# Performance work log

Hardware: AMD Instinct MI355X
Metric: run time of the kernel (lower is better)

Reference implementation:

```python
import jax, jax.numpy as jnp
import numpy as np

N = 50000
EPS = 1e-4
NUM_CLASSES = 10
PROTOS_PER_CLASS = 5


def setup_inputs() -> dict:
    key = jax.random.key(0)
    ks = jax.random.split(key, 12)
    x = jax.random.normal(ks[0], (N, 512), dtype=jnp.float32)
    edge_index = jax.random.randint(ks[1], (2, 640000), 0, N, dtype=jnp.int64)
    # GCNConv weights (PyG: y = x @ W^T + b after aggregation)
    def glorot(k, o, i):
        s = jnp.sqrt(6.0 / (o + i)).astype(jnp.float32)
        return jax.random.uniform(k, (o, i), jnp.float32, -s, s)
    W1 = glorot(ks[2], 128, 512); b1 = jnp.zeros((128,), jnp.float32)
    W2 = glorot(ks[3], 128, 128); b2 = jnp.zeros((128,), jnp.float32)
    W3 = glorot(ks[4], 128, 128); b3 = jnp.zeros((128,), jnp.float32)
    prototype_vectors = jax.random.uniform(ks[5], (NUM_CLASSES * PROTOS_PER_CLASS, 128), jnp.float32)
    # last layer: +1 for prototype's own class, -0.5 elsewhere, no bias
    proto_class = jnp.arange(NUM_CLASSES * PROTOS_PER_CLASS) // PROTOS_PER_CLASS  # [P]
    identity = (proto_class[None, :] == jnp.arange(NUM_CLASSES)[:, None]).astype(jnp.float32)  # [C,P]
    last_w = 1.0 * identity + (-0.5) * (1.0 - identity)
    return {"x": x, "edge_index": edge_index, "W1": W1, "b1": b1, "W2": W2,
            "b2": b2, "W3": W3, "b3": b3,
            "prototype_vectors": prototype_vectors, "last_w": last_w}


def _gcn_conv(h, src, dst, deg_inv_sqrt, W, b):
    # h: [N,Fin]; messages from src -> dst with symmetric norm; self-loops included in src/dst
    m = h @ W.T                                   # [N,Fout]
    norm = deg_inv_sqrt[src] * deg_inv_sqrt[dst]  # [E+N]
    out = jax.ops.segment_sum(norm[:, None] * m[src], dst, num_segments=N)
    return out + b


def reference(x, edge_index, W1, b1, W2, b2, W3, b3, prototype_vectors, last_w):
    # add self loops once; degree computed on targets (PyG gcn_norm)
    loop = jnp.arange(N, dtype=edge_index.dtype)
    src = jnp.concatenate([edge_index[0], loop])
    dst = jnp.concatenate([edge_index[1], loop])
    deg = jax.ops.segment_sum(jnp.ones_like(src, dtype=x.dtype), dst, num_segments=N)
    deg_inv_sqrt = jnp.where(deg > 0, jax.lax.rsqrt(deg), 0.0)

    h = jax.nn.relu(_gcn_conv(x, src, dst, deg_inv_sqrt, W1, b1))
    h = jax.nn.relu(_gcn_conv(h, src, dst, deg_inv_sqrt, W2, b2))
    h = jax.nn.relu(_gcn_conv(h, src, dst, deg_inv_sqrt, W3, b3))
    emb = h  # [N,128]

    xp = emb @ prototype_vectors.T                                    # [N,P]
    distance = (-2.0 * xp + jnp.sum(emb * emb, axis=1, keepdims=True)
                + jnp.sum(prototype_vectors * prototype_vectors, axis=1)[None, :])
    similarity = jnp.log((distance + 1.0) / (distance + EPS))         # [N,P]
    logits = similarity @ last_w.T                                    # [N,C]
    probs = jax.nn.softmax(logits, axis=-1)
    return logits, probs, emb, distance
```

## Files before the change

kernel.cpp:

```cpp
#include <hip/hip_runtime.h>
#include <cstdint>
#include <cstddef>

#define NFEAT 128
#define NPROTO 50
#define NCLS 10

typedef __attribute__((ext_vector_type(8))) short short8;
typedef __attribute__((ext_vector_type(4))) float floatx4;
typedef _Float16 halfv8 __attribute__((ext_vector_type(8)));


__device__ __forceinline__ void split1(float v, unsigned short& h, unsigned short& l) {
  unsigned int b = __float_as_uint(v);
  h = (unsigned short)(b >> 16);
  float r = v - __uint_as_float(b & 0xFFFF0000u);
  l = (unsigned short)(__float_as_uint(r) >> 16);
}


__global__ __launch_bounds__(256)
void prep_kernel(const float* __restrict__ W1, const float* __restrict__ W2,
                 const float* __restrict__ W3, const float* __restrict__ proto,
                 unsigned short* __restrict__ W1h, unsigned short* __restrict__ W1l,
                 unsigned short* __restrict__ W2h, unsigned short* __restrict__ W2l,
                 unsigned short* __restrict__ W3h, unsigned short* __restrict__ W3l,
                 unsigned short* __restrict__ Ph, unsigned short* __restrict__ Pl,
                 float* __restrict__ pn, int* __restrict__ zero_base, int zero_n) {
  int g = blockIdx.x * 256 + threadIdx.x;
  int stride = gridDim.x * 256;
  for (int i = g; i < 128 * 512; i += stride) {
    unsigned short h, l; split1(W1[i], h, l); W1h[i] = h; W1l[i] = l;
  }
  for (int i = g; i < 128 * 128; i += stride) {
    unsigned short h, l; split1(W2[i], h, l); W2h[i] = h; W2l[i] = l;
  }
  for (int i = g; i < 128 * 128; i += stride) {
    unsigned short h, l; split1(W3[i], h, l); W3h[i] = h; W3l[i] = l;
  }
  for (int i = g; i < 64 * 128; i += stride) {
    int p = i >> 7;
    float v = (p < NPROTO) ? proto[p * 128 + (i & 127)] : 0.f;
    unsigned short h, l; split1(v, h, l); Ph[i] = h; Pl[i] = l;
  }
  for (int i = g; i < zero_n; i += stride) zero_base[i] = 0;
  if (g < 64) {
    float s = 0.f;
    if (g < NPROTO)
      for (int f = 0; f < 128; ++f) { float v = proto[g * 128 + f]; s += v * v; }
    pn[g] = s;
  }
}


__global__ __launch_bounds__(256) void count_kernel(const int* __restrict__ dst,
                                                    int* __restrict__ cnt, int E) {
  int e = blockIdx.x * 256 + threadIdx.x;
  if (e < E) atomicAdd(&cnt[dst[e]], 1);
}


__global__ __launch_bounds__(256)
void scan_lb_kernel(const int* __restrict__ cnt, int* __restrict__ row_ptr,
                    float* __restrict__ dis,
                    unsigned long long* __restrict__ state, int Nn) {
  __shared__ int s[256];
  __shared__ int exc_s;
  int b = blockIdx.x;
  int t = threadIdx.x;
  int i = b * 256 + t;
  int v = (i < Nn) ? cnt[i] : 0;
  s[t] = v;
  __syncthreads();
#pragma unroll
  for (int off = 1; off < 256; off <<= 1) {
    int add = (t >= off) ? s[t - off] : 0;
    __syncthreads();
    s[t] += add;
    __syncthreads();
  }
  int tile_sum = s[255];
  if (t == 0) {
    unsigned long long pkt = (1ULL << 32) | (unsigned int)tile_sum;
    __hip_atomic_store(&state[b], pkt, __ATOMIC_RELEASE, __HIP_MEMORY_SCOPE_AGENT);
    if (b == 0) exc_s = 0;
  }
  if (b > 0 && t < 64) {
    int acc = 0;
    for (int p = t; p < b; p += 64) {
      unsigned long long pk;
      do {
        pk = __hip_atomic_load(&state[p], __ATOMIC_ACQUIRE, __HIP_MEMORY_SCOPE_AGENT);
      } while ((pk >> 32) == 0);
      acc += (int)(unsigned int)pk;
    }
#pragma unroll
    for (int off = 32; off; off >>= 1) acc += __shfl_down(acc, off);
    if (t == 0) exc_s = acc;
  }
  __syncthreads();
  int exc = exc_s;
  if (i < Nn) {
    row_ptr[i] = exc + s[t] - v;
    dis[i] = 1.0f / sqrtf((float)(v + 1));
  }
  if (b == gridDim.x - 1 && t == 0) row_ptr[Nn] = exc + tile_sum;
}

__global__ __launch_bounds__(256) void fill_kernel(const int* __restrict__ src,
                                                   const int* __restrict__ dst,
                                                   const int* __restrict__ row_ptr,
                                                   int* __restrict__ cursor,
                                                   int* __restrict__ csr_src, int E) {
  int e = blockIdx.x * 256 + threadIdx.x;
  if (e < E) {
    int d = dst[e];
    int pos = atomicAdd(&cursor[d], 1);
    csr_src[row_ptr[d] + pos] = src[e];
  }
}


__global__ __launch_bounds__(512, 2)
void gemm_p1(const float* __restrict__ A, const float* __restrict__ dis,
             const unsigned short* __restrict__ Wh, const unsigned short* __restrict__ Wl,
             _Float16* __restrict__ C, int M) {
  __shared__ short8 Wlds[4096];
  int t = threadIdx.x;
  int w = t >> 6, lane = t & 63;
  int col = lane & 15, quad = lane >> 4;
  int ntiles = (M + 15) >> 4;
  int tile = blockIdx.x * 8 + w;
  if (tile >= ntiles) tile = ntiles - 1;
  int m0 = tile * 16;

  floatx4 acc[8];
#pragma unroll
  for (int b = 0; b < 8; ++b) acc[b] = floatx4{0.f, 0.f, 0.f, 0.f};

  int r = m0 + col;
  int row = r < M ? r : M - 1;
  float dsc = dis[row];

  for (int p = 0; p < 4; ++p) {
    const int kb = p * 128;
    __syncthreads();
#pragma unroll
    for (int i = 0; i < 8; ++i) {
      int u = i * 512 + t;
      int pl_ = u >> 11;
      int v = u & 2047;
      int g = v >> 8, q = (v >> 4) & 15, c = v & 15;
      const unsigned short* srcp = (pl_ ? Wl : Wh) + (size_t)(g * 16 + c) * 512 + kb + q * 8;
      __builtin_amdgcn_global_load_lds(
          (const __attribute__((address_space(1))) void*)srcp,
          (__attribute__((address_space(3))) void*)((char*)Wlds + (size_t)(i * 512 + w * 64) * 16),
          16, 0, 0);
    }
    float4 pf[4][2];
#pragma unroll
    for (int c0 = 0; c0 < 4; ++c0) {
      const float* pp = A + (size_t)row * 512 + kb + c0 * 32 + quad * 8;
      pf[c0][0] = *(const float4*)pp;
      pf[c0][1] = *(const float4*)(pp + 4);
    }
    __syncthreads();

#pragma unroll
    for (int ck = 0; ck < 4; ++ck) {
      float4 va = pf[ck][0];
      float4 vb = pf[ck][1];
      float f[8] = {va.x, va.y, va.z, va.w, vb.x, vb.y, vb.z, vb.w};
      short8 ah, al;
#pragma unroll
      for (int j = 0; j < 8; ++j) {
        unsigned short h, l;
        split1(f[j] * dsc, h, l);
        ah[j] = (short)h; al[j] = (short)l;
      }
#pragma unroll
      for (int nt = 0; nt < 8; ++nt) {
        int u = nt * 256 + (ck * 4 + quad) * 16 + col;
        short8 bh = Wlds[u];
        short8 bl = Wlds[2048 + u];
        acc[nt] = __builtin_amdgcn_mfma_f32_16x16x32_bf16(ah, bh, acc[nt], 0, 0, 0);
        acc[nt] = __builtin_amdgcn_mfma_f32_16x16x32_bf16(al, bh, acc[nt], 0, 0, 0);
        acc[nt] = __builtin_amdgcn_mfma_f32_16x16x32_bf16(ah, bl, acc[nt], 0, 0, 0);
      }
    }
  }

#pragma unroll
  for (int rr = 0; rr < 4; ++rr) {
    int m = m0 + quad * 4 + rr;
    if (m < M) {
#pragma unroll
      for (int nt = 0; nt < 8; ++nt)
        C[(size_t)m * NFEAT + nt * 16 + col] = (_Float16)acc[nt][rr];
    }
  }
}


__global__ __launch_bounds__(512, 2)
void gemm_p2(const unsigned short* __restrict__ Ah, const unsigned short* __restrict__ Al,
             const unsigned short* __restrict__ Wh, const unsigned short* __restrict__ Wl,
             _Float16* __restrict__ C, int M) {
  __shared__ short8 Wlds[4096];
  int t = threadIdx.x;
  int w = t >> 6, lane = t & 63;
  int col = lane & 15, quad = lane >> 4;
  int ntiles = (M + 31) >> 5;
  int tile = blockIdx.x * 8 + w;
  if (tile >= ntiles) tile = ntiles - 1;
  int m0 = tile * 32;

  floatx4 acc[2][8];
#pragma unroll
  for (int a = 0; a < 2; ++a)
#pragma unroll
    for (int b = 0; b < 8; ++b) acc[a][b] = floatx4{0.f, 0.f, 0.f, 0.f};

  int row[2];
#pragma unroll
  for (int mt = 0; mt < 2; ++mt) {
    int r = m0 + mt * 16 + col;
    row[mt] = r < M ? r : M - 1;
  }

#pragma unroll
  for (int i = 0; i < 4; ++i) {
    int u = i * 512 + t;
    int g = u >> 8, q = (u >> 4) & 15, c = u & 15;
    size_t off = (size_t)(g * 16 + c) * 128 + q * 8;
    char* dst = (char*)Wlds + (size_t)(i * 512 + w * 64) * 16;
    __builtin_amdgcn_global_load_lds(
        (const __attribute__((address_space(1))) void*)(Wh + off),
        (__attribute__((address_space(3))) void*)dst, 16, 0, 0);
    __builtin_amdgcn_global_load_lds(
        (const __attribute__((address_space(1))) void*)(Wl + off),
        (__attribute__((address_space(3))) void*)(dst + 32768), 16, 0, 0);
  }

  short8 pah[4][2], pal[4][2];
#pragma unroll
  for (int ck = 0; ck < 4; ++ck)
#pragma unroll
    for (int mt = 0; mt < 2; ++mt) {
      size_t off = (size_t)row[mt] * 128 + ck * 32 + quad * 8;
      pah[ck][mt] = *(const short8*)(Ah + off);
      pal[ck][mt] = *(const short8*)(Al + off);
    }

  __syncthreads();

#pragma unroll
  for (int ck = 0; ck < 4; ++ck) {
#pragma unroll
    for (int nt = 0; nt < 8; ++nt) {
      int u = (nt * 16 + ck * 4 + quad) * 16 + col;
      short8 bh = Wlds[u];
      short8 bl = Wlds[2048 + u];
#pragma unroll
      for (int mt = 0; mt < 2; ++mt) {
        acc[mt][nt] = __builtin_amdgcn_mfma_f32_16x16x32_bf16(pah[ck][mt], bh, acc[mt][nt], 0, 0, 0);
        acc[mt][nt] = __builtin_amdgcn_mfma_f32_16x16x32_bf16(pal[ck][mt], bh, acc[mt][nt], 0, 0, 0);
        acc[mt][nt] = __builtin_amdgcn_mfma_f32_16x16x32_bf16(pah[ck][mt], bl, acc[mt][nt], 0, 0, 0);
      }
    }
  }

#pragma unroll
  for (int mt = 0; mt < 2; ++mt)
#pragma unroll
    for (int r = 0; r < 4; ++r) {
      int m = m0 + mt * 16 + quad * 4 + r;
      if (m < M) {
#pragma unroll
        for (int nt = 0; nt < 8; ++nt)
          C[(size_t)m * NFEAT + nt * 16 + col] = (_Float16)acc[mt][nt][r];
      }
    }
}


template<int MODE>
__global__ __launch_bounds__(256)
void agg_kernel(const _Float16* __restrict__ m, const int* __restrict__ row_ptr,
                const int* __restrict__ csr_src, const float* __restrict__ dis,
                const float* __restrict__ bias,
                unsigned int* __restrict__ out_h, unsigned int* __restrict__ out_l,
                float* __restrict__ out_f, int Nn) {
  int t = threadIdx.x;
  int w = t >> 6, lane = t & 63;
  int sub = lane >> 4, l = lane & 15;
  int i = blockIdx.x * 16 + w * 4 + sub;
  if (i >= Nn) return;
  const halfv8* m8 = (const halfv8*)m;
  halfv8 sv = m8[(size_t)i * 16 + l];
  float acc[8];
#pragma unroll
  for (int j = 0; j < 8; ++j) acc[j] = (float)sv[j];
  int e0 = row_ptr[i], e1 = row_ptr[i + 1];
  int e = e0;
  for (; e + 4 <= e1; e += 4) {
    int s0 = csr_src[e], s1 = csr_src[e + 1], s2 = csr_src[e + 2], s3 = csr_src[e + 3];
    halfv8 v0 = m8[(size_t)s0 * 16 + l];
    halfv8 v1 = m8[(size_t)s1 * 16 + l];
    halfv8 v2 = m8[(size_t)s2 * 16 + l];
    halfv8 v3 = m8[(size_t)s3 * 16 + l];
#pragma unroll
    for (int j = 0; j < 8; ++j)
      acc[j] += ((float)v0[j] + (float)v1[j]) + ((float)v2[j] + (float)v3[j]);
  }
  for (; e < e1; ++e) {
    int s = csr_src[e];
    halfv8 v = m8[(size_t)s * 16 + l];
#pragma unroll
    for (int j = 0; j < 8; ++j) acc[j] += (float)v[j];
  }
  float di = dis[i];
  float4 ba = ((const float4*)bias)[l * 2];
  float4 bb = ((const float4*)bias)[l * 2 + 1];
  float bv[8] = {ba.x, ba.y, ba.z, ba.w, bb.x, bb.y, bb.z, bb.w};
  float r[8];
#pragma unroll
  for (int j = 0; j < 8; ++j) r[j] = fmaxf(fmaf(di, acc[j], bv[j]), 0.f);
  if (MODE == 0) {
    unsigned int ph[4], pl[4];
#pragma unroll
    for (int j = 0; j < 4; ++j) {
      unsigned short h0, l0, h1, l1;
      split1(di * r[2 * j], h0, l0);
      split1(di * r[2 * j + 1], h1, l1);
      ph[j] = (unsigned int)h0 | ((unsigned int)h1 << 16);
      pl[j] = (unsigned int)l0 | ((unsigned int)l1 << 16);
    }
    ((uint4*)out_h)[(size_t)i * 16 + l] = make_uint4(ph[0], ph[1], ph[2], ph[3]);
    ((uint4*)out_l)[(size_t)i * 16 + l] = make_uint4(pl[0], pl[1], pl[2], pl[3]);
  } else {
    ((float4*)out_f)[(size_t)i * 32 + l * 2] = make_float4(r[0], r[1], r[2], r[3]);
    ((float4*)out_f)[(size_t)i * 32 + l * 2 + 1] = make_float4(r[4], r[5], r[6], r[7]);
  }
}


__global__ __launch_bounds__(256)
void proto_mfma(const float* __restrict__ emb,
                const unsigned short* __restrict__ Ph, const unsigned short* __restrict__ Pl,
                const float* __restrict__ pn, const float* __restrict__ lastw,
                float* __restrict__ out_logits, float* __restrict__ out_probs,
                float* __restrict__ out_dist, int Nn) {
  __shared__ float simS[64][65];
  int t = threadIdx.x;
  int w = t >> 6, lane = t & 63;
  int col = lane & 15, quad = lane >> 4;
  int m0 = blockIdx.x * 64 + w * 16;
  int row = m0 + col;
  int r0 = row < Nn ? row : Nn - 1;

  floatx4 acc[4];
#pragma unroll
  for (int nt = 0; nt < 4; ++nt) acc[nt] = floatx4{0.f, 0.f, 0.f, 0.f};

  float en = 0.f;
  const float* ap = emb + (size_t)r0 * 128 + quad * 8;
#pragma unroll
  for (int kc = 0; kc < 4; ++kc) {
    float4 va = *(const float4*)(ap + kc * 32);
    float4 vb = *(const float4*)(ap + kc * 32 + 4);
    float f[8] = {va.x, va.y, va.z, va.w, vb.x, vb.y, vb.z, vb.w};
    short8 ah, al;
#pragma unroll
    for (int j = 0; j < 8; ++j) {
      unsigned short h, l;
      split1(f[j], h, l);
      ah[j] = (short)h; al[j] = (short)l;
      en = fmaf(f[j], f[j], en);
    }
#pragma unroll
    for (int nt = 0; nt < 4; ++nt) {
      const unsigned short* bp = Ph + (size_t)(nt * 16 + col) * 128 + kc * 32 + quad * 8;
      const unsigned short* bq = Pl + (size_t)(nt * 16 + col) * 128 + kc * 32 + quad * 8;
      short8 bh = *(const short8*)bp;
      short8 bl = *(const short8*)bq;
      acc[nt] = __builtin_amdgcn_mfma_f32_16x16x32_bf16(ah, bh, acc[nt], 0, 0, 0);
      acc[nt] = __builtin_amdgcn_mfma_f32_16x16x32_bf16(al, bh, acc[nt], 0, 0, 0);
      acc[nt] = __builtin_amdgcn_mfma_f32_16x16x32_bf16(ah, bl, acc[nt], 0, 0, 0);
    }
  }
  en += __shfl_xor(en, 16);
  en += __shfl_xor(en, 32);

  float pnv[4];
#pragma unroll
  for (int nt = 0; nt < 4; ++nt) pnv[nt] = pn[nt * 16 + col];

#pragma unroll
  for (int r = 0; r < 4; ++r) {
    int node = m0 + quad * 4 + r;
    float enr = __shfl(en, quad * 4 + r);
    bool valid = node < Nn;
#pragma unroll
    for (int nt = 0; nt < 4; ++nt) {
      int p = nt * 16 + col;
      float d = enr - 2.f * acc[nt][r] + pnv[nt];
      float sim = (p < NPROTO) ? logf((d + 1.0f) / (d + 1e-4f)) : 0.f;
      simS[w * 16 + quad * 4 + r][p] = sim;
      if (valid && p < NPROTO) out_dist[(size_t)node * NPROTO + p] = d;
    }
  }
  __syncthreads();

  if (t < 64) {
    int node = blockIdx.x * 64 + t;
    if (node < Nn) {
      float sims[NPROTO];
#pragma unroll
      for (int p = 0; p < NPROTO; ++p) sims[p] = simS[t][p];
      float lg[NCLS];
      float mx = -1e30f;
#pragma unroll
      for (int c = 0; c < NCLS; ++c) {
        float s = 0.f;
#pragma unroll
        for (int p = 0; p < NPROTO; ++p) s = fmaf(sims[p], lastw[c * NPROTO + p], s);
        lg[c] = s;
        mx = fmaxf(mx, s);
      }
      float ss = 0.f;
#pragma unroll
      for (int c = 0; c < NCLS; ++c) ss += expf(lg[c] - mx);
      float inv = 1.f / ss;
#pragma unroll
      for (int c = 0; c < NCLS; ++c) {
        out_logits[(size_t)node * NCLS + c] = lg[c];
        out_probs[(size_t)node * NCLS + c] = expf(lg[c] - mx) * inv;
      }
    }
  }
}


extern "C" void kernel_launch(void* const* d_in, const int* in_sizes, int n_in,
                              void* d_out, int out_size, void* d_ws, size_t ws_size,
                              hipStream_t stream) {
  const float* x    = (const float*)d_in[0];
  const int*  eidx  = (const int*)d_in[1];
  const float* W1   = (const float*)d_in[2];
  const float* b1   = (const float*)d_in[3];
  const float* W2   = (const float*)d_in[4];
  const float* b2   = (const float*)d_in[5];
  const float* W3   = (const float*)d_in[6];
  const float* b3   = (const float*)d_in[7];
  const float* prot = (const float*)d_in[8];
  const float* lastw= (const float*)d_in[9];

  const int Nn = in_sizes[0] / 512;
  const int E  = in_sizes[1] / 2;
  const int* esrc = eidx;
  const int* edst = eidx + E;

  float* out        = (float*)d_out;
  float* out_logits = out;
  float* out_probs  = out + (size_t)Nn * NCLS;
  float* out_emb    = out + (size_t)Nn * 2 * NCLS;
  float* out_dist   = out_emb + (size_t)Nn * NFEAT;

  _Float16* mbuf = (_Float16*)d_ws;
  unsigned int* hh = (unsigned int*)(mbuf + (size_t)Nn * NFEAT);
  unsigned int* hl = hh + (size_t)Nn * 64;
  unsigned short* W1h = (unsigned short*)(hl + (size_t)Nn * 64);
  unsigned short* W1l = W1h + 128 * 512;
  unsigned short* W2h = W1l + 128 * 512;
  unsigned short* W2l = W2h + 128 * 128;
  unsigned short* W3h = W2l + 128 * 128;
  unsigned short* W3l = W3h + 128 * 128;
  unsigned short* Ph  = W3l + 128 * 128;
  unsigned short* Pl  = Ph + 64 * 128;
  float* pn    = (float*)(Pl + 64 * 128);
  unsigned long long* state = (unsigned long long*)(pn + 64);
  int* cnt     = (int*)(state + 256);
  int* cursor  = cnt + Nn;
  float* dis   = (float*)(cursor + Nn);
  int* row_ptr = (int*)(dis + Nn);
  int* csr_src = row_ptr + Nn + 1;

  const int nb = (Nn + 255) / 256;
  const int zero_n = 512 + 2 * Nn;

  prep_kernel<<<128, 256, 0, stream>>>(W1, W2, W3, prot, W1h, W1l, W2h, W2l,
                                       W3h, W3l, Ph, Pl, pn, (int*)state, zero_n);
  count_kernel<<<(E + 255) / 256, 256, 0, stream>>>(edst, cnt, E);
  scan_lb_kernel<<<nb, 256, 0, stream>>>(cnt, row_ptr, dis, state, Nn);
  fill_kernel<<<(E + 255) / 256, 256, 0, stream>>>(esrc, edst, row_ptr, cursor, csr_src, E);

  int ntiles16 = (Nn + 15) / 16;
  int p1blocks = (ntiles16 + 7) / 8;
  int ntiles32 = (Nn + 31) / 32;
  int gblocks = (ntiles32 + 7) / 8;
  int ablocks = (Nn + 15) / 16;
  gemm_p1<<<p1blocks, 512, 0, stream>>>(x, dis, W1h, W1l, mbuf, Nn);
  agg_kernel<0><<<ablocks, 256, 0, stream>>>(mbuf, row_ptr, csr_src, dis, b1, hh, hl, nullptr, Nn);
  gemm_p2<<<gblocks, 512, 0, stream>>>((const unsigned short*)hh, (const unsigned short*)hl,
                                       W2h, W2l, mbuf, Nn);
  agg_kernel<0><<<ablocks, 256, 0, stream>>>(mbuf, row_ptr, csr_src, dis, b2, hh, hl, nullptr, Nn);
  gemm_p2<<<gblocks, 512, 0, stream>>>((const unsigned short*)hh, (const unsigned short*)hl,
                                       W3h, W3l, mbuf, Nn);
  agg_kernel<1><<<ablocks, 256, 0, stream>>>(mbuf, row_ptr, csr_src, dis, b3, nullptr, nullptr, out_emb, Nn);

  proto_mfma<<<(Nn + 63) / 64, 256, 0, stream>>>(out_emb, Ph, Pl, pn, lastw,
                                                 out_logits, out_probs, out_dist, Nn);
}
```

Measured before the change: 397.8 us.

## Split feature matrices into 32-column chunks so aggregation gathers fit in cache

The GEMM outputs and the hidden-state hi/lo buffers are stored as four column-major chunks of 32 features instead of row-major 128 features. The aggregation kernel now runs one grid slice per chunk, with 4 lanes per node instead of 16. Each gather pass then touches a smaller working set (N×32 halves), which aims to raise L2/MALL hit rates for the random neighbor reads. The cost is that the CSR row pointers and indices are read four times, and each row gather is only 64 bytes.

```diff
diff --git a/kernel.cpp b/kernel.cpp
--- a/kernel.cpp
+++ b/kernel.cpp
@@ -190,13 +190,15 @@
     }
   }
 
+  size_t cstride = (size_t)M * 32;
 #pragma unroll
   for (int rr = 0; rr < 4; ++rr) {
     int m = m0 + quad * 4 + rr;
     if (m < M) {
 #pragma unroll
       for (int nt = 0; nt < 8; ++nt)
-        C[(size_t)m * NFEAT + nt * 16 + col] = (_Float16)acc[nt][rr];
+        C[(size_t)(nt >> 1) * cstride + (size_t)m * 32 + (nt & 1) * 16 + col] =
+            (_Float16)acc[nt][rr];
     }
   }
 }
@@ -242,12 +244,13 @@
         (__attribute__((address_space(3))) void*)(dst + 32768), 16, 0, 0);
   }
 
+  size_t cstride = (size_t)M * 32;
   short8 pah[4][2], pal[4][2];
 #pragma unroll
   for (int ck = 0; ck < 4; ++ck)
 #pragma unroll
     for (int mt = 0; mt < 2; ++mt) {
-      size_t off = (size_t)row[mt] * 128 + ck * 32 + quad * 8;
+      size_t off = (size_t)ck * cstride + (size_t)row[mt] * 32 + quad * 8;
       pah[ck][mt] = *(const short8*)(Ah + off);
       pal[ck][mt] = *(const short8*)(Al + off);
     }
@@ -278,7 +281,8 @@
       if (m < M) {
 #pragma unroll
         for (int nt = 0; nt < 8; ++nt)
-          C[(size_t)m * NFEAT + nt * 16 + col] = (_Float16)acc[mt][nt][r];
+          C[(size_t)(nt >> 1) * cstride + (size_t)m * 32 + (nt & 1) * 16 + col] =
+              (_Float16)acc[mt][nt][r];
       }
     }
 }
@@ -290,42 +294,47 @@
                 const int* __restrict__ csr_src, const float* __restrict__ dis,
                 const float* __restrict__ bias,
                 unsigned int* __restrict__ out_h, unsigned int* __restrict__ out_l,
-                float* __restrict__ out_f, int Nn) {
+                float* __restrict__ out_f, int Nn, int nblk) {
   int t = threadIdx.x;
-  int w = t >> 6, lane = t & 63;
-  int sub = lane >> 4, l = lane & 15;
-  int i = blockIdx.x * 16 + w * 4 + sub;
-  if (i >= Nn) return;
-  const halfv8* m8 = (const halfv8*)m;
-  halfv8 sv = m8[(size_t)i * 16 + l];
+  int bid = blockIdx.x;
+  int chunk = bid / nblk;
+  int nb = bid - chunk * nblk;
+  int node = nb * 64 + (t >> 2);
+  int l2 = t & 3;
+  if (node >= Nn) return;
+  const halfv8* m8 = (const halfv8*)(m + (size_t)chunk * Nn * 32);
+
+  halfv8 sv = m8[(size_t)node * 4 + l2];
   float acc[8];
 #pragma unroll
   for (int j = 0; j < 8; ++j) acc[j] = (float)sv[j];
-  int e0 = row_ptr[i], e1 = row_ptr[i + 1];
-  int e = e0;
+
+  int e = row_ptr[node], e1 = row_ptr[node + 1];
   for (; e + 4 <= e1; e += 4) {
     int s0 = csr_src[e], s1 = csr_src[e + 1], s2 = csr_src[e + 2], s3 = csr_src[e + 3];
-    halfv8 v0 = m8[(size_t)s0 * 16 + l];
-    halfv8 v1 = m8[(size_t)s1 * 16 + l];
-    halfv8 v2 = m8[(size_t)s2 * 16 + l];
-    halfv8 v3 = m8[(size_t)s3 * 16 + l];
+    halfv8 v0 = m8[(size_t)s0 * 4 + l2];
+    halfv8 v1 = m8[(size_t)s1 * 4 + l2];
+    halfv8 v2 = m8[(size_t)s2 * 4 + l2];
+    halfv8 v3 = m8[(size_t)s3 * 4 + l2];
 #pragma unroll
     for (int j = 0; j < 8; ++j)
       acc[j] += ((float)v0[j] + (float)v1[j]) + ((float)v2[j] + (float)v3[j]);
   }
   for (; e < e1; ++e) {
-    int s = csr_src[e];
-    halfv8 v = m8[(size_t)s * 16 + l];
+    halfv8 v = m8[(size_t)csr_src[e] * 4 + l2];
 #pragma unroll
     for (int j = 0; j < 8; ++j) acc[j] += (float)v[j];
   }
-  float di = dis[i];
-  float4 ba = ((const float4*)bias)[l * 2];
-  float4 bb = ((const float4*)bias)[l * 2 + 1];
+
+  float di = dis[node];
+  const float* bp = bias + chunk * 32 + l2 * 8;
+  float4 ba = *(const float4*)bp;
+  float4 bb = *(const float4*)(bp + 4);
   float bv[8] = {ba.x, ba.y, ba.z, ba.w, bb.x, bb.y, bb.z, bb.w};
   float r[8];
 #pragma unroll
   for (int j = 0; j < 8; ++j) r[j] = fmaxf(fmaf(di, acc[j], bv[j]), 0.f);
+
   if (MODE == 0) {
     unsigned int ph[4], pl[4];
 #pragma unroll
@@ -336,11 +345,13 @@
       ph[j] = (unsigned int)h0 | ((unsigned int)h1 << 16);
       pl[j] = (unsigned int)l0 | ((unsigned int)l1 << 16);
     }
-    ((uint4*)out_h)[(size_t)i * 16 + l] = make_uint4(ph[0], ph[1], ph[2], ph[3]);
-    ((uint4*)out_l)[(size_t)i * 16 + l] = make_uint4(pl[0], pl[1], pl[2], pl[3]);
+    size_t o = (size_t)chunk * Nn * 4 + (size_t)node * 4 + l2;
+    ((uint4*)out_h)[o] = make_uint4(ph[0], ph[1], ph[2], ph[3]);
+    ((uint4*)out_l)[o] = make_uint4(pl[0], pl[1], pl[2], pl[3]);
   } else {
-    ((float4*)out_f)[(size_t)i * 32 + l * 2] = make_float4(r[0], r[1], r[2], r[3]);
-    ((float4*)out_f)[(size_t)i * 32 + l * 2 + 1] = make_float4(r[4], r[5], r[6], r[7]);
+    float* op = out_f + (size_t)node * 128 + chunk * 32 + l2 * 8;
+    *(float4*)op = make_float4(r[0], r[1], r[2], r[3]);
+    *(float4*)(op + 4) = make_float4(r[4], r[5], r[6], r[7]);
   }
 }
 
@@ -499,15 +510,16 @@
   int p1blocks = (ntiles16 + 7) / 8;
   int ntiles32 = (Nn + 31) / 32;
   int gblocks = (ntiles32 + 7) / 8;
-  int ablocks = (Nn + 15) / 16;
+  int anblk = (Nn + 63) / 64;
+  int ablocks = 4 * anblk;
   gemm_p1<<<p1blocks, 512, 0, stream>>>(x, dis, W1h, W1l, mbuf, Nn);
-  agg_kernel<0><<<ablocks, 256, 0, stream>>>(mbuf, row_ptr, csr_src, dis, b1, hh, hl, nullptr, Nn);
+  agg_kernel<0><<<ablocks, 256, 0, stream>>>(mbuf, row_ptr, csr_src, dis, b1, hh, hl, nullptr, Nn, anblk);
   gemm_p2<<<gblocks, 512, 0, stream>>>((const unsigned short*)hh, (const unsigned short*)hl,
                                        W2h, W2l, mbuf, Nn);
-  agg_kernel<0><<<ablocks, 256, 0, stream>>>(mbuf, row_ptr, csr_src, dis, b2, hh, hl, nullptr, Nn);
+  agg_kernel<0><<<ablocks, 256, 0, stream>>>(mbuf, row_ptr, csr_src, dis, b2, hh, hl, nullptr, Nn, anblk);
   gemm_p2<<<gblocks, 512, 0, stream>>>((const unsigned short*)hh, (const unsigned short*)hl,
                                        W3h, W3l, mbuf, Nn);
-  agg_kernel<1><<<ablocks, 256, 0, stream>>>(mbuf, row_ptr, csr_src, dis, b3, nullptr, nullptr, out_emb, Nn);
+  agg_kernel<1><<<ablocks, 256, 0, stream>>>(mbuf, row_ptr, csr_src, dis, b3, nullptr, nullptr, out_emb, Nn, anblk);
 
   proto_mfma<<<(Nn + 63) / 64, 256, 0, stream>>>(out_emb, Ph, Pl, pn, lastw,
                                                  out_logits, out_probs, out_dist, Nn);
```

New measurement: 419.4 us. 1.05x slower.
